# Optimization experiments

Hardware: AMD Instinct MI355X
Metric: run time of the kernel (lower is better)

The kernel has to match this reference:

```python
import jax, jax.numpy as jnp
import numpy as np

B, T, C, H = 4, 2048, 1024, 16
HS = C // H  # head_size = 64
FF = 4 * C   # 4096
EPS = 1e-5


def _layernorm(x, g, b):
    mu = jnp.mean(x, axis=-1, keepdims=True)
    var = jnp.mean(jnp.square(x - mu), axis=-1, keepdims=True)
    return (x - mu) * jax.lax.rsqrt(var + EPS) * g + b


def setup_inputs() -> dict:
    key = jax.random.key(0)
    ks = jax.random.split(key, 12)
    s_in = 1.0 / np.sqrt(C)
    s_ff = 1.0 / np.sqrt(FF)
    return {
        "x": jax.random.normal(ks[0], (B, T, C), jnp.float32),
        # per-head projection weights stacked: [H, C, HS]
        "Wq": jax.random.normal(ks[1], (H, C, HS), jnp.float32) * s_in,
        "Wk": jax.random.normal(ks[2], (H, C, HS), jnp.float32) * s_in,
        "Wv": jax.random.normal(ks[3], (H, C, HS), jnp.float32) * s_in,
        "Wo": jax.random.normal(ks[4], (C, C), jnp.float32) * s_in,
        "bo": jnp.zeros((C,), jnp.float32),
        "g1": jnp.ones((C,), jnp.float32),
        "b1": jnp.zeros((C,), jnp.float32),
        "g2": jnp.ones((C,), jnp.float32),
        "b2": jnp.zeros((C,), jnp.float32),
        "W1": jax.random.normal(ks[5], (C, FF), jnp.float32) * s_in,
        "bf1": jnp.zeros((FF,), jnp.float32),
        "W2": jax.random.normal(ks[6], (FF, C), jnp.float32) * s_ff,
        "bf2": jnp.zeros((C,), jnp.float32),
    }


def reference(x, Wq, Wk, Wv, Wo, bo, g1, b1, g2, b2, W1, bf1, W2, bf2):
    # pre-norm
    h = _layernorm(x, g1, b1)                       # [B,T,C]
    q = jnp.einsum('btc,hcd->bhtd', h, Wq)          # [B,H,T,HS]
    k = jnp.einsum('btc,hcd->bhtd', h, Wk)
    v = jnp.einsum('btc,hcd->bhtd', h, Wv)
    w = jnp.einsum('bhtd,bhsd->bhts', q, k) * (HS ** -0.5)  # [B,H,T,S]
    mask = jnp.tril(jnp.ones((T, T), bool))          # causal tril
    w = jnp.where(mask[None, None], w, -jnp.inf)
    # NB: original code softmaxes over dim=1 of [B,T,T], i.e. the QUERY axis
    w = jax.nn.softmax(w, axis=-2)
    o = jnp.einsum('bhts,bhsd->bhtd', w, v)          # [B,H,T,HS]
    o = jnp.transpose(o, (0, 2, 1, 3)).reshape(B, T, C)  # concat heads
    x = x + o @ Wo + bo                              # residual 1 (dropout=0)
    f = _layernorm(x, g2, b2)
    ff = jax.nn.relu(f @ W1 + bf1) @ W2 + bf2        # FFN (dropout=0)
    return x + ff
```

## Files before the change

### kernel.cpp

```cpp
#include <hip/hip_runtime.h>
#include <hip/hip_bf16.h>


#define T_SEQ 2048
#define SCALE2 0.1803368801f

typedef __attribute__((ext_vector_type(8))) short short8;
typedef __attribute__((ext_vector_type(4))) float f32x4;

typedef __attribute__((address_space(1))) unsigned int g_u32;
typedef __attribute__((address_space(3))) unsigned int l_u32;

__device__ __forceinline__ unsigned short f2bf(float f) {
  __hip_bfloat16 h = __float2bfloat16(f);
  union { __hip_bfloat16 h; unsigned short u; } x; x.h = h;
  return x.u;
}
__device__ __forceinline__ float bf2f(unsigned short u) {
  union { unsigned u; float f; } x; x.u = (unsigned)u << 16;
  return x.f;
}

__device__ __forceinline__ void g2lds16(const void* g, void* l) {
  __builtin_amdgcn_global_load_lds((g_u32*)g, (l_u32*)l, 16, 0, 0);
}

__device__ __forceinline__ int xcd_swz(int flat, int nwg) {
  if ((nwg & 7) != 0) return flat;
  return (flat & 7) * (nwg >> 3) + (flat >> 3);
}

template <int EPI, int BN, int NSTG>
__global__ __launch_bounds__(512, 2) void gemm256(
    const unsigned short* __restrict__ A, const unsigned short* __restrict__ Bt,
    int M, int N, int K,
    unsigned short* __restrict__ out16, float* __restrict__ outF,
    const float* __restrict__ bias, const float* __restrict__ resid) {
  constexpr int PM = (BN == 128) ? 4 : 2;
  constexpr int PN = 8 / PM;
  constexpr int WM = 256 / PM;
  constexpr int FM = WM / 16;
  constexpr int WN = BN / PN;
  constexpr int FN = WN / 16;
  constexpr int NB = (BN * 8) / 512;
  constexpr int NL = 4 + NB;
  extern __shared__ unsigned short lds[];
  unsigned short* ldsA = lds;
  unsigned short* ldsB = lds + NSTG * 16384;
  const int tid = threadIdx.x, lane = tid & 63, wid = tid >> 6;
  const int wm = wid / PN, wn = wid % PN;
  const int nx = gridDim.x;
  const int flat = blockIdx.y * nx + blockIdx.x;
  const int swz = xcd_swz(flat, nx * gridDim.y);
  const int mBase = (swz / nx) * 256, nBase = (swz % nx) * BN;

  f32x4 acc[FM][FN];
#pragma unroll
  for (int i = 0; i < FM; ++i)
#pragma unroll
    for (int j = 0; j < FN; ++j)
#pragma unroll
      for (int e = 0; e < 4; ++e) acc[i][j][e] = 0.f;

  auto stage = [&](int buf, int kt) {
    const int k0 = kt << 6;
#pragma unroll
    for (int it = 0; it < 4; ++it) {
      int g = it * 512 + tid;
      int row = g >> 3, colL = g & 7;
      int col = colL ^ (row & 7);
      g2lds16(A + ((size_t)(mBase + row) * K + k0 + col * 8),
              &ldsA[buf * 16384 + (it * 512 + wid * 64) * 8]);
    }
#pragma unroll
    for (int it = 0; it < NB; ++it) {
      int g = it * 512 + tid;
      int row = g >> 3, colL = g & 7;
      int col = colL ^ (row & 7);
      g2lds16(Bt + ((size_t)(nBase + row) * K + k0 + col * 8),
              &ldsB[buf * (BN * 64) + (it * 512 + wid * 64) * 8]);
    }
  };

  const int nKT = K >> 6;
#pragma unroll
  for (int i = 0; i < NSTG; ++i) stage(i, i);
  asm volatile("s_waitcnt vmcnt(%0)" ::"n"((NSTG - 1) * NL) : "memory");
  __builtin_amdgcn_sched_barrier(0);
  __builtin_amdgcn_s_barrier();
  __builtin_amdgcn_sched_barrier(0);

  for (int kt = 0; kt < nKT; ++kt) {
    const int cur = kt % NSTG;
    short8 bf[FN][2];
#pragma unroll
    for (int fn = 0; fn < FN; ++fn)
#pragma unroll
      for (int ks = 0; ks < 2; ++ks) {
        int r = wn * WN + fn * 16 + (lane & 15);
        int c = (ks * 4 + (lane >> 4)) ^ (r & 7);
        bf[fn][ks] = *(const short8*)&ldsB[cur * (BN * 64) + r * 64 + c * 8];
      }
#pragma unroll
    for (int mf = 0; mf < FM; ++mf) {
      short8 af[2];
#pragma unroll
      for (int ks = 0; ks < 2; ++ks) {
        int r = wm * WM + mf * 16 + (lane & 15);
        int c = (ks * 4 + (lane >> 4)) ^ (r & 7);
        af[ks] = *(const short8*)&ldsA[cur * 16384 + r * 64 + c * 8];
      }
      __builtin_amdgcn_s_setprio(1);
#pragma unroll
      for (int fn = 0; fn < FN; ++fn)
#pragma unroll
        for (int ks = 0; ks < 2; ++ks)
          acc[mf][fn] = __builtin_amdgcn_mfma_f32_16x16x32_bf16(
              af[ks], bf[fn][ks], acc[mf][fn], 0, 0, 0);
      __builtin_amdgcn_s_setprio(0);
    }
    if (kt + 1 < nKT) {
      asm volatile("s_waitcnt lgkmcnt(0)" ::: "memory");
      __builtin_amdgcn_sched_barrier(0);
      __builtin_amdgcn_s_barrier();
      __builtin_amdgcn_sched_barrier(0);
      if (kt + NSTG < nKT) {
        stage(cur, kt + NSTG);
        asm volatile("s_waitcnt vmcnt(%0)" ::"n"((NSTG - 1) * NL) : "memory");
      } else if (NSTG == 3 && kt + 2 < nKT) {
        asm volatile("s_waitcnt vmcnt(%0)" ::"n"(NL) : "memory");
      } else {
        asm volatile("s_waitcnt vmcnt(0)" ::: "memory");
      }
      __builtin_amdgcn_sched_barrier(0);
      __builtin_amdgcn_s_barrier();
      __builtin_amdgcn_sched_barrier(0);
    }
  }

#pragma unroll
  for (int am = 0; am < FM; ++am)
#pragma unroll
    for (int fn = 0; fn < FN; ++fn) {
      int col = nBase + wn * WN + fn * 16 + (lane & 15);
      int row0 = mBase + wm * WM + am * 16 + ((lane >> 4) << 2);
      if (EPI == 0) {
#pragma unroll
        for (int r = 0; r < 4; ++r)
          out16[(size_t)(row0 + r) * N + col] = f2bf(acc[am][fn][r]);
      } else if (EPI == 1) {
        float bv = bias[col];
#pragma unroll
        for (int r = 0; r < 4; ++r) {
          size_t idx = (size_t)(row0 + r) * N + col;
          outF[idx] = acc[am][fn][r] + bv + resid[idx];
        }
      } else {
        float bv = bias[col];
#pragma unroll
        for (int r = 0; r < 4; ++r)
          out16[(size_t)(row0 + r) * N + col] =
              f2bf(fmaxf(acc[am][fn][r] + bv, 0.f));
      }
    }
}

__global__ __launch_bounds__(256) void ln_bf16(
    const float* __restrict__ x, const float* __restrict__ gw,
    const float* __restrict__ bw, unsigned short* __restrict__ out) {
  __shared__ float red[8];
  const int row = blockIdx.x, tid = threadIdx.x;
  const float4 v = ((const float4*)(x + (size_t)row * 1024))[tid];
  float s = v.x + v.y + v.z + v.w;
  float q = v.x * v.x + v.y * v.y + v.z * v.z + v.w * v.w;
#pragma unroll
  for (int off = 32; off >= 1; off >>= 1) {
    s += __shfl_down(s, off);
    q += __shfl_down(q, off);
  }
  const int lane = tid & 63, wid = tid >> 6;
  if (lane == 0) { red[wid] = s; red[4 + wid] = q; }
  __syncthreads();
  float S = red[0] + red[1] + red[2] + red[3];
  float Q = red[4] + red[5] + red[6] + red[7];
  float mu = S * (1.f / 1024.f);
  float var = Q * (1.f / 1024.f) - mu * mu;
  float rs = rsqrtf(var + 1e-5f);
  int c = tid * 4;
  ushort4 ov;
  ov.x = f2bf((v.x - mu) * rs * gw[c + 0] + bw[c + 0]);
  ov.y = f2bf((v.y - mu) * rs * gw[c + 1] + bw[c + 1]);
  ov.z = f2bf((v.z - mu) * rs * gw[c + 2] + bw[c + 2]);
  ov.w = f2bf((v.w - mu) * rs * gw[c + 3] + bw[c + 3]);
  *(ushort4*)&out[(size_t)row * 1024 + c] = ov;
}

__global__ __launch_bounds__(256) void pack_qkv(
    const float* __restrict__ Wq, const float* __restrict__ Wk,
    const float* __restrict__ Wv, unsigned short* __restrict__ out) {
  __shared__ float tile[64 * 65];
  const int tid = threadIdx.x;
  const float* W = (blockIdx.z == 0) ? Wq : (blockIdx.z == 1) ? Wk : Wv;
  const int h = blockIdx.y, r0 = blockIdx.x * 64;
#pragma unroll
  for (int it = 0; it < 4; ++it) {
    int e4 = it * 256 + tid;
    int r = e4 >> 4, c4 = e4 & 15;
    float4 v = *(const float4*)&W[((size_t)h * 1024 + r0 + r) * 64 + c4 * 4];
    tile[r * 65 + c4 * 4 + 0] = v.x;
    tile[r * 65 + c4 * 4 + 1] = v.y;
    tile[r * 65 + c4 * 4 + 2] = v.z;
    tile[r * 65 + c4 * 4 + 3] = v.w;
  }
  __syncthreads();
#pragma unroll
  for (int it = 0; it < 4; ++it) {
    int e4 = it * 256 + tid;
    int d = e4 >> 4, r4 = e4 & 15;
    ushort4 ov;
    ov.x = f2bf(tile[(r4 * 4 + 0) * 65 + d]);
    ov.y = f2bf(tile[(r4 * 4 + 1) * 65 + d]);
    ov.z = f2bf(tile[(r4 * 4 + 2) * 65 + d]);
    ov.w = f2bf(tile[(r4 * 4 + 3) * 65 + d]);
    *(ushort4*)&out[(size_t)(blockIdx.z * 1024 + h * 64 + d) * 1024 + r0 +
                    r4 * 4] = ov;
  }
}

__global__ __launch_bounds__(256) void transpose_cast(
    const float* __restrict__ in, unsigned short* __restrict__ out, int R,
    int C) {
  __shared__ float tile[64 * 65];
  const int tid = threadIdx.x;
  const int r0 = blockIdx.x * 64, c0 = blockIdx.y * 64;
#pragma unroll
  for (int it = 0; it < 4; ++it) {
    int e4 = it * 256 + tid;
    int r = e4 >> 4, c4 = e4 & 15;
    float4 v = *(const float4*)&in[(size_t)(r0 + r) * C + c0 + c4 * 4];
    tile[r * 65 + c4 * 4 + 0] = v.x;
    tile[r * 65 + c4 * 4 + 1] = v.y;
    tile[r * 65 + c4 * 4 + 2] = v.z;
    tile[r * 65 + c4 * 4 + 3] = v.w;
  }
  __syncthreads();
#pragma unroll
  for (int it = 0; it < 4; ++it) {
    int e4 = it * 256 + tid;
    int c = e4 >> 4, r4 = e4 & 15;
    ushort4 ov;
    ov.x = f2bf(tile[(r4 * 4 + 0) * 65 + c]);
    ov.y = f2bf(tile[(r4 * 4 + 1) * 65 + c]);
    ov.z = f2bf(tile[(r4 * 4 + 2) * 65 + c]);
    ov.w = f2bf(tile[(r4 * 4 + 3) * 65 + c]);
    *(ushort4*)&out[(size_t)(c0 + c) * R + r0 + r4 * 4] = ov;
  }
}

__global__ __launch_bounds__(256) void vtrans(
    const unsigned short* __restrict__ qkv, const float* __restrict__ lpart,
    unsigned short* __restrict__ vT) {
  __shared__ unsigned short tile[64 * 66];
  const int tid = threadIdx.x;
  const int bh = blockIdx.y, b = bh >> 4, h = bh & 15;
  const int t0 = blockIdx.x * 64;
#pragma unroll
  for (int it = 0; it < 8; ++it) {
    int e2 = it * 256 + tid;
    int r = e2 >> 5, c2 = e2 & 31;
    unsigned v = *(const unsigned*)&qkv[(size_t)(b * T_SEQ + t0 + r) * 3072 +
                                        2048 + h * 64 + c2 * 2];
    float l0 = lpart[(size_t)bh * T_SEQ + t0 + r];
    float l1 = lpart[(size_t)(64 + bh) * T_SEQ + t0 + r];
    float li = 1.f / (l0 + l1);
    unsigned short lo = f2bf(bf2f((unsigned short)(v & 0xffff)) * li);
    unsigned short hi = f2bf(bf2f((unsigned short)(v >> 16)) * li);
    *(unsigned*)&tile[r * 66 + c2 * 2] = (unsigned)lo | ((unsigned)hi << 16);
  }
  __syncthreads();
#pragma unroll
  for (int it = 0; it < 8; ++it) {
    int e2 = it * 256 + tid;
    int d = e2 >> 5, t2 = e2 & 31;
    unsigned short a = tile[(t2 * 2) * 66 + d];
    unsigned short bb = tile[(t2 * 2 + 1) * 66 + d];
    unsigned pk = (unsigned)a | ((unsigned)bb << 16);
    *(unsigned*)&vT[(size_t)(bh * 64 + d) * T_SEQ + t0 + t2 * 2] = pk;
  }
}

__global__ __launch_bounds__(256, 4) void attn_stats(
    const unsigned short* __restrict__ qkv, float* __restrict__ lpart) {
  __shared__ unsigned short qt[4][2][32 * 64];
  __shared__ float redL[4][2][64];
  const int tid = threadIdx.x, lane = tid & 63, w = tid >> 6;
  const int f = xcd_swz(blockIdx.y * 32 + blockIdx.x, 2048);
  const int half = f & 1, px = (f >> 1) & 15, bh = f >> 5;
  const int b = bh >> 4, h = bh & 15;
  const int sxA = px, sxB = 31 - px;
  const int sA = sxA * 64, sB = sxB * 64;
  const int m = half * 4 + w;

  short8 kfA[4][2], kfB[4][2];
#pragma unroll
  for (int fn = 0; fn < 4; ++fn)
#pragma unroll
    for (int ks = 0; ks < 2; ++ks) {
      int d = 1024 + h * 64 + ks * 32 + ((lane >> 4) << 3);
      kfA[fn][ks] = *(const short8*)&qkv[(size_t)(b * T_SEQ + sA + fn * 16 +
                                                  (lane & 15)) * 3072 + d];
      kfB[fn][ks] = *(const short8*)&qkv[(size_t)(b * T_SEQ + sB + fn * 16 +
                                                  (lane & 15)) * 3072 + d];
    }
  float lA[4] = {0.f, 0.f, 0.f, 0.f}, lB[4] = {0.f, 0.f, 0.f, 0.f};

  auto stageQ = [&](int buf, int idx) {
    int t0 = idx * 32;
#pragma unroll
    for (int it = 0; it < 4; ++it) {
      int g = it * 64 + lane;
      int row = g >> 3;
      int col = (g & 7) ^ (row & 7);
      g2lds16(qkv + ((size_t)(b * T_SEQ + t0 + row) * 3072 + h * 64 + col * 8),
              &qt[w][buf][it * 512]);
    }
  };

  auto accum = [&](const short8 (&af)[2], const short8 (&kf)[4][2],
                   float (&lacc)[4], int sBase, int tRow, bool diag) {
    f32x4 sc[4];
#pragma unroll
    for (int fn = 0; fn < 4; ++fn)
#pragma unroll
      for (int e = 0; e < 4; ++e) sc[fn][e] = 0.f;
    __builtin_amdgcn_s_setprio(1);
#pragma unroll
    for (int fn = 0; fn < 4; ++fn)
#pragma unroll
      for (int ks = 0; ks < 2; ++ks)
        sc[fn] = __builtin_amdgcn_mfma_f32_16x16x32_bf16(af[ks], kf[fn][ks],
                                                         sc[fn], 0, 0, 0);
    __builtin_amdgcn_s_setprio(0);
    if (diag) {
#pragma unroll
      for (int fn = 0; fn < 4; ++fn) {
        int s = sBase + fn * 16 + (lane & 15);
        float e0 = (tRow + 0 >= s) ? exp2f(sc[fn][0] * SCALE2) : 0.f;
        float e1 = (tRow + 1 >= s) ? exp2f(sc[fn][1] * SCALE2) : 0.f;
        float e2 = (tRow + 2 >= s) ? exp2f(sc[fn][2] * SCALE2) : 0.f;
        float e3 = (tRow + 3 >= s) ? exp2f(sc[fn][3] * SCALE2) : 0.f;
        lacc[fn] += (e0 + e1) + (e2 + e3);
      }
    } else {
#pragma unroll
      for (int fn = 0; fn < 4; ++fn) {
        float e0 = exp2f(sc[fn][0] * SCALE2);
        float e1 = exp2f(sc[fn][1] * SCALE2);
        float e2 = exp2f(sc[fn][2] * SCALE2);
        float e3 = exp2f(sc[fn][3] * SCALE2);
        lacc[fn] += (e0 + e1) + (e2 + e3);
      }
    }
  };

  const int d0 = 2 * sxA - m;
  const int fi = m + (d0 > 0 ? (((d0 + 7) >> 3) << 3) : 0);
  int cur = 0;
  if (fi < 64) stageQ(0, fi);
  for (int idx = fi; idx < 64; idx += 8, cur ^= 1) {
    if (idx + 8 < 64) {
      stageQ(cur ^ 1, idx + 8);
      asm volatile("s_waitcnt vmcnt(4)" ::: "memory");
    } else {
      asm volatile("s_waitcnt vmcnt(0)" ::: "memory");
    }
    const int t0g = idx * 32;
    const bool doB = idx >= 2 * sxB;
#pragma unroll
    for (int mf = 0; mf < 2; ++mf) {
      short8 af[2];
#pragma unroll
      for (int ks = 0; ks < 2; ++ks) {
        int r = mf * 16 + (lane & 15);
        int c = (ks * 4 + (lane >> 4)) ^ (r & 7);
        af[ks] = *(const short8*)&qt[w][cur][r * 64 + c * 8];
      }
      int tRow = t0g + mf * 16 + ((lane >> 4) << 2);
      accum(af, kfA, lA, sA, tRow, idx <= 2 * sxA + 1);
      if (doB) accum(af, kfB, lB, sB, tRow, idx <= 2 * sxB + 1);
    }
  }
#pragma unroll
  for (int fn = 0; fn < 4; ++fn) {
    lA[fn] += __shfl_down(lA[fn], 32);
    lA[fn] += __shfl_down(lA[fn], 16);
    lB[fn] += __shfl_down(lB[fn], 32);
    lB[fn] += __shfl_down(lB[fn], 16);
  }
  if (lane < 16) {
#pragma unroll
    for (int fn = 0; fn < 4; ++fn) {
      redL[w][0][fn * 16 + lane] = lA[fn];
      redL[w][1][fn * 16 + lane] = lB[fn];
    }
  }
  __syncthreads();
  if (tid < 128) {
    int which = tid >> 6;
    float l = redL[0][which][lane] + redL[1][which][lane] +
              redL[2][which][lane] + redL[3][which][lane];
    int sbase = (which == 0) ? sA : sB;
    lpart[((size_t)half * 64 + bh) * T_SEQ + sbase + lane] = l;
  }
}

__global__ __launch_bounds__(256, 2) void attn_pv(
    const unsigned short* __restrict__ qkv, const unsigned short* __restrict__ vT,
    unsigned short* __restrict__ o) {
  __shared__ unsigned short kbuf[2][64 * 64];
  __shared__ unsigned short vbuf[2][64 * 64];
  __shared__ unsigned short pl[128 * 64];
  const int tid = threadIdx.x, lane = tid & 63, wid = tid >> 6;
  const int f = xcd_swz(blockIdx.y * 8 + blockIdx.x, 512);
  const int bx = f & 7, bh = f >> 3;
  const int b = bh >> 4, h = bh & 15;
  const int tA = bx * 128, tB = (15 - bx) * 128;
  const int nSTA = 2 * bx + 2, nSTB = 32 - 2 * bx;

  short8 qfA[2][2], qfB[2][2];
#pragma unroll
  for (int mf = 0; mf < 2; ++mf)
#pragma unroll
    for (int ks = 0; ks < 2; ++ks) {
      int d = h * 64 + ks * 32 + ((lane >> 4) << 3);
      int rloc = wid * 32 + mf * 16 + (lane & 15);
      qfA[mf][ks] =
          *(const short8*)&qkv[(size_t)(b * T_SEQ + tA + rloc) * 3072 + d];
      qfB[mf][ks] =
          *(const short8*)&qkv[(size_t)(b * T_SEQ + tB + rloc) * 3072 + d];
    }
  f32x4 oaccA[2][4], oaccB[2][4];
#pragma unroll
  for (int i = 0; i < 2; ++i)
#pragma unroll
    for (int j = 0; j < 4; ++j)
#pragma unroll
      for (int e = 0; e < 4; ++e) { oaccA[i][j][e] = 0.f; oaccB[i][j][e] = 0.f; }

  auto stage = [&](int buf, int st) {
#pragma unroll
    for (int it = 0; it < 2; ++it) {
      int g = it * 256 + tid;
      int row = g >> 3, colL = g & 7;
      int col = colL ^ (row & 7);
      g2lds16(qkv + ((size_t)(b * T_SEQ + st * 64 + row) * 3072 + 1024 +
                     h * 64 + col * 8),
              &kbuf[buf][(it * 256 + wid * 64) * 8]);
      g2lds16(vT + ((size_t)(bh * 64 + row) * T_SEQ + st * 64 + col * 8),
              &vbuf[buf][(it * 256 + wid * 64) * 8]);
    }
  };

  auto qkstore = [&](const short8 (&qf)[2][2], int tBase, int s0,
                     bool maskNeeded, int cur) {
    f32x4 sc[4][2];
#pragma unroll
    for (int i = 0; i < 4; ++i)
#pragma unroll
      for (int j = 0; j < 2; ++j)
#pragma unroll
        for (int e = 0; e < 4; ++e) sc[i][j][e] = 0.f;
    __builtin_amdgcn_s_setprio(1);
#pragma unroll
    for (int fn = 0; fn < 4; ++fn)
#pragma unroll
      for (int ks = 0; ks < 2; ++ks) {
        int r = fn * 16 + (lane & 15);
        int c = (ks * 4 + (lane >> 4)) ^ (r & 7);
        short8 kfr = *(const short8*)&kbuf[cur][r * 64 + c * 8];
        sc[fn][0] = __builtin_amdgcn_mfma_f32_16x16x32_bf16(kfr, qf[0][ks],
                                                            sc[fn][0], 0, 0, 0);
        sc[fn][1] = __builtin_amdgcn_mfma_f32_16x16x32_bf16(kfr, qf[1][ks],
                                                            sc[fn][1], 0, 0, 0);
      }
    __builtin_amdgcn_s_setprio(0);
#pragma unroll
    for (int mf = 0; mf < 2; ++mf) {
      int tl = wid * 32 + mf * 16 + (lane & 15);
      int tG = tBase + tl;
#pragma unroll
      for (int fn = 0; fn < 4; ++fn) {
        int sl = fn * 16 + ((lane >> 4) << 2);
        float p0 = exp2f(sc[fn][mf][0] * SCALE2);
        float p1 = exp2f(sc[fn][mf][1] * SCALE2);
        float p2 = exp2f(sc[fn][mf][2] * SCALE2);
        float p3 = exp2f(sc[fn][mf][3] * SCALE2);
        if (maskNeeded) {
          int sG = s0 + sl;
          p0 = (tG >= sG + 0) ? p0 : 0.f;
          p1 = (tG >= sG + 1) ? p1 : 0.f;
          p2 = (tG >= sG + 2) ? p2 : 0.f;
          p3 = (tG >= sG + 3) ? p3 : 0.f;
        }
        uint2 pk;
        pk.x = (unsigned)f2bf(p0) | ((unsigned)f2bf(p1) << 16);
        pk.y = (unsigned)f2bf(p2) | ((unsigned)f2bf(p3) << 16);
        int byteoff = tl * 128 + ((sl * 2) ^ ((tl & 7) << 4));
        *(uint2*)((char*)pl + byteoff) = pk;
      }
    }
  };

  auto pvphase = [&](f32x4 (&oacc)[2][4], int cur) {
    __builtin_amdgcn_s_setprio(1);
#pragma unroll
    for (int ks = 0; ks < 2; ++ks) {
      short8 pa[2];
#pragma unroll
      for (int mf = 0; mf < 2; ++mf) {
        int rowa = wid * 32 + mf * 16 + (lane & 15);
        int kb = ks * 64 + ((lane >> 4) << 4);
        pa[mf] = *(const short8*)((const char*)pl + rowa * 128 +
                                  (kb ^ ((rowa & 7) << 4)));
      }
#pragma unroll
      for (int df = 0; df < 4; ++df) {
        int r = df * 16 + (lane & 15);
        int c = (ks * 4 + (lane >> 4)) ^ (r & 7);
        short8 vb = *(const short8*)&vbuf[cur][r * 64 + c * 8];
        oacc[0][df] = __builtin_amdgcn_mfma_f32_16x16x32_bf16(pa[0], vb,
                                                              oacc[0][df], 0, 0, 0);
        oacc[1][df] = __builtin_amdgcn_mfma_f32_16x16x32_bf16(pa[1], vb,
                                                              oacc[1][df], 0, 0, 0);
      }
    }
    __builtin_amdgcn_s_setprio(0);
  };

  auto bar_lgkm = [&]() {
    asm volatile("s_waitcnt lgkmcnt(0)" ::: "memory");
    __builtin_amdgcn_sched_barrier(0);
    __builtin_amdgcn_s_barrier();
    __builtin_amdgcn_sched_barrier(0);
  };

  stage(0, 0);
  asm volatile("s_waitcnt vmcnt(0)" ::: "memory");
  __builtin_amdgcn_sched_barrier(0);
  __builtin_amdgcn_s_barrier();
  __builtin_amdgcn_sched_barrier(0);

  int cur = 0;
  for (int st = 0; st < nSTB; ++st) {
    const int s0 = st * 64;
    const bool doA = st < nSTA;

    if (st + 1 < nSTB) stage(cur ^ 1, st + 1);

    if (doA) {
      qkstore(qfA, tA, s0, st >= nSTA - 2, cur);
      bar_lgkm();
      pvphase(oaccA, cur);
      bar_lgkm();
    }
    qkstore(qfB, tB, s0, st >= nSTB - 2, cur);
    bar_lgkm();
    pvphase(oaccB, cur);
    asm volatile("s_waitcnt vmcnt(0) lgkmcnt(0)" ::: "memory");
    __builtin_amdgcn_sched_barrier(0);
    __builtin_amdgcn_s_barrier();
    __builtin_amdgcn_sched_barrier(0);
    cur ^= 1;
  }
#pragma unroll
  for (int mf = 0; mf < 2; ++mf)
#pragma unroll
    for (int df = 0; df < 4; ++df) {
      int d = h * 64 + df * 16 + (lane & 15);
      int ra = tA + wid * 32 + mf * 16 + ((lane >> 4) << 2);
      int rb = tB + wid * 32 + mf * 16 + ((lane >> 4) << 2);
#pragma unroll
      for (int r = 0; r < 4; ++r) {
        o[(size_t)(b * T_SEQ + ra + r) * 1024 + d] = f2bf(oaccA[mf][df][r]);
        o[(size_t)(b * T_SEQ + rb + r) * 1024 + d] = f2bf(oaccB[mf][df][r]);
      }
    }
}

extern "C" void kernel_launch(void* const* d_in, const int* in_sizes, int n_in,
                              void* d_out, int out_size, void* d_ws,
                              size_t ws_size, hipStream_t stream) {
  const float* x = (const float*)d_in[0];
  const float* Wq = (const float*)d_in[1];
  const float* Wk = (const float*)d_in[2];
  const float* Wv = (const float*)d_in[3];
  const float* Wo = (const float*)d_in[4];
  const float* bo = (const float*)d_in[5];
  const float* g1 = (const float*)d_in[6];
  const float* b1 = (const float*)d_in[7];
  const float* g2 = (const float*)d_in[8];
  const float* b2 = (const float*)d_in[9];
  const float* W1 = (const float*)d_in[10];
  const float* bf1 = (const float*)d_in[11];
  const float* W2 = (const float*)d_in[12];
  const float* bf2 = (const float*)d_in[13];
  float* out = (float*)d_out;

  char* ws = (char*)d_ws;
  size_t off = 0;
  auto alloc = [&](size_t bytes) {
    char* p = ws + off;
    off += (bytes + 255) & ~(size_t)255;
    return p;
  };
  unsigned short* Wqkv = (unsigned short*)alloc(3072ull * 1024 * 2);
  unsigned short* WoT = (unsigned short*)alloc(1024ull * 1024 * 2);
  unsigned short* W1T = (unsigned short*)alloc(4096ull * 1024 * 2);
  unsigned short* W2T = (unsigned short*)alloc(1024ull * 4096 * 2);
  unsigned short* hbuf = (unsigned short*)alloc(8192ull * 1024 * 2);
  char* regionE = alloc(8192ull * 3072 * 2 + 64ull * 64 * 2048 * 2);
  unsigned short* qkv = (unsigned short*)regionE;
  unsigned short* vT = (unsigned short*)(regionE + 8192ull * 3072 * 2);
  unsigned short* act = (unsigned short*)regionE;
  float* lbuf = (float*)alloc(128ull * 2048 * 4);
  float* x1 = (float*)alloc(8192ull * 1024 * 4);
  unsigned short* fbuf = (unsigned short*)alloc(8192ull * 1024 * 2);
  unsigned short* obuf = hbuf;

  (void)in_sizes; (void)n_in; (void)out_size; (void)ws_size;

  const size_t LDS128_3 = 3 * (16384 + 8192) * 2;
  const size_t LDS256_2 = 2 * (16384 + 16384) * 2;

  pack_qkv<<<dim3(16, 16, 3), 256, 0, stream>>>(Wq, Wk, Wv, Wqkv);
  transpose_cast<<<dim3(16, 16), 256, 0, stream>>>(Wo, WoT, 1024, 1024);
  transpose_cast<<<dim3(16, 64), 256, 0, stream>>>(W1, W1T, 1024, 4096);
  transpose_cast<<<dim3(64, 16), 256, 0, stream>>>(W2, W2T, 4096, 1024);
  ln_bf16<<<8192, 256, 0, stream>>>(x, g1, b1, hbuf);
  gemm256<0, 128, 3><<<dim3(24, 32), 512, LDS128_3, stream>>>(
      hbuf, Wqkv, 8192, 3072, 1024, qkv, nullptr, nullptr, nullptr);
  attn_stats<<<dim3(32, 64), 256, 0, stream>>>(qkv, lbuf);
  vtrans<<<dim3(32, 64), 256, 0, stream>>>(qkv, lbuf, vT);
  attn_pv<<<dim3(8, 64), 256, 0, stream>>>(qkv, vT, obuf);
  gemm256<1, 128, 3><<<dim3(8, 32), 512, LDS128_3, stream>>>(
      obuf, WoT, 8192, 1024, 1024, nullptr, x1, bo, x);
  ln_bf16<<<8192, 256, 0, stream>>>(x1, g2, b2, fbuf);
  gemm256<2, 256, 2><<<dim3(16, 32), 512, LDS256_2, stream>>>(
      fbuf, W1T, 8192, 4096, 1024, act, nullptr, bf1, nullptr);
  gemm256<1, 128, 3><<<dim3(8, 32), 512, LDS128_3, stream>>>(
      act, W2T, 8192, 1024, 4096, nullptr, out, bf2, x1);
}
```

Before: 435.6 us.

## Split paired causal attention blocks into single-tile blocks and use 2-stage GEMM pipelines

The attn_pv kernel no longer pairs a short and a long causal query tile in one block to balance work. Each block now handles one 128-row query tile, the grid doubles to 1024 blocks, and blocks are ordered longest-first so the scheduler can balance load dynamically. Separately, the 128-wide GEMM instantiations drop from 3 to 2 pipeline stages, which shrinks LDS use and may allow more occupancy at the cost of less latency hiding.

After: 451.2 us. +3.6%, slower.

```diff
diff --git a/kernel.cpp b/kernel.cpp
--- a/kernel.cpp
+++ b/kernel.cpp
@@ -421,31 +421,29 @@
   __shared__ unsigned short vbuf[2][64 * 64];
   __shared__ unsigned short pl[128 * 64];
   const int tid = threadIdx.x, lane = tid & 63, wid = tid >> 6;
-  const int f = xcd_swz(blockIdx.y * 8 + blockIdx.x, 512);
-  const int bx = f & 7, bh = f >> 3;
+  const int f = xcd_swz(blockIdx.y * 16 + blockIdx.x, 1024);
+  const int bx = 15 - (f & 15), bh = f >> 4;
   const int b = bh >> 4, h = bh & 15;
-  const int tA = bx * 128, tB = (15 - bx) * 128;
-  const int nSTA = 2 * bx + 2, nSTB = 32 - 2 * bx;
-
-  short8 qfA[2][2], qfB[2][2];
+  const int tA = bx * 128;
+  const int nST = 2 * bx + 2;
+
+  short8 qf[2][2];
 #pragma unroll
   for (int mf = 0; mf < 2; ++mf)
 #pragma unroll
     for (int ks = 0; ks < 2; ++ks) {
       int d = h * 64 + ks * 32 + ((lane >> 4) << 3);
       int rloc = wid * 32 + mf * 16 + (lane & 15);
-      qfA[mf][ks] =
+      qf[mf][ks] =
           *(const short8*)&qkv[(size_t)(b * T_SEQ + tA + rloc) * 3072 + d];
-      qfB[mf][ks] =
-          *(const short8*)&qkv[(size_t)(b * T_SEQ + tB + rloc) * 3072 + d];
-    }
-  f32x4 oaccA[2][4], oaccB[2][4];
+    }
+  f32x4 oacc[2][4];
 #pragma unroll
   for (int i = 0; i < 2; ++i)
 #pragma unroll
     for (int j = 0; j < 4; ++j)
 #pragma unroll
-      for (int e = 0; e < 4; ++e) { oaccA[i][j][e] = 0.f; oaccB[i][j][e] = 0.f; }
+      for (int e = 0; e < 4; ++e) oacc[i][j][e] = 0.f;
 
   auto stage = [&](int buf, int st) {
 #pragma unroll
@@ -461,8 +459,7 @@
     }
   };
 
-  auto qkstore = [&](const short8 (&qf)[2][2], int tBase, int s0,
-                     bool maskNeeded, int cur) {
+  auto qkstore = [&](int s0, bool maskNeeded, int cur) {
     f32x4 sc[4][2];
 #pragma unroll
     for (int i = 0; i < 4; ++i)
@@ -487,7 +484,7 @@
 #pragma unroll
     for (int mf = 0; mf < 2; ++mf) {
       int tl = wid * 32 + mf * 16 + (lane & 15);
-      int tG = tBase + tl;
+      int tG = tA + tl;
 #pragma unroll
       for (int fn = 0; fn < 4; ++fn) {
         int sl = fn * 16 + ((lane >> 4) << 2);
@@ -511,7 +508,7 @@
     }
   };
 
-  auto pvphase = [&](f32x4 (&oacc)[2][4], int cur) {
+  auto pvphase = [&](int cur) {
     __builtin_amdgcn_s_setprio(1);
 #pragma unroll
     for (int ks = 0; ks < 2; ++ks) {
@@ -537,13 +534,6 @@
     __builtin_amdgcn_s_setprio(0);
   };
 
-  auto bar_lgkm = [&]() {
-    asm volatile("s_waitcnt lgkmcnt(0)" ::: "memory");
-    __builtin_amdgcn_sched_barrier(0);
-    __builtin_amdgcn_s_barrier();
-    __builtin_amdgcn_sched_barrier(0);
-  };
-
   stage(0, 0);
   asm volatile("s_waitcnt vmcnt(0)" ::: "memory");
   __builtin_amdgcn_sched_barrier(0);
@@ -551,21 +541,15 @@
   __builtin_amdgcn_sched_barrier(0);
 
   int cur = 0;
-  for (int st = 0; st < nSTB; ++st) {
-    const int s0 = st * 64;
-    const bool doA = st < nSTA;
-
-    if (st + 1 < nSTB) stage(cur ^ 1, st + 1);
-
-    if (doA) {
-      qkstore(qfA, tA, s0, st >= nSTA - 2, cur);
-      bar_lgkm();
-      pvphase(oaccA, cur);
-      bar_lgkm();
-    }
-    qkstore(qfB, tB, s0, st >= nSTB - 2, cur);
-    bar_lgkm();
-    pvphase(oaccB, cur);
+  for (int st = 0; st < nST; ++st) {
+    if (st + 1 < nST) stage(cur ^ 1, st + 1);
+
+    qkstore(st * 64, st >= nST - 2, cur);
+    asm volatile("s_waitcnt lgkmcnt(0)" ::: "memory");
+    __builtin_amdgcn_sched_barrier(0);
+    __builtin_amdgcn_s_barrier();
+    __builtin_amdgcn_sched_barrier(0);
+    pvphase(cur);
     asm volatile("s_waitcnt vmcnt(0) lgkmcnt(0)" ::: "memory");
     __builtin_amdgcn_sched_barrier(0);
     __builtin_amdgcn_s_barrier();
@@ -578,12 +562,9 @@
     for (int df = 0; df < 4; ++df) {
       int d = h * 64 + df * 16 + (lane & 15);
       int ra = tA + wid * 32 + mf * 16 + ((lane >> 4) << 2);
-      int rb = tB + wid * 32 + mf * 16 + ((lane >> 4) << 2);
-#pragma unroll
-      for (int r = 0; r < 4; ++r) {
-        o[(size_t)(b * T_SEQ + ra + r) * 1024 + d] = f2bf(oaccA[mf][df][r]);
-        o[(size_t)(b * T_SEQ + rb + r) * 1024 + d] = f2bf(oaccB[mf][df][r]);
-      }
+#pragma unroll
+      for (int r = 0; r < 4; ++r)
+        o[(size_t)(b * T_SEQ + ra + r) * 1024 + d] = f2bf(oacc[mf][df][r]);
     }
 }
 
@@ -629,7 +610,7 @@
 
   (void)in_sizes; (void)n_in; (void)out_size; (void)ws_size;
 
-  const size_t LDS128_3 = 3 * (16384 + 8192) * 2;
+  const size_t LDS128_2 = 2 * (16384 + 8192) * 2;
   const size_t LDS256_2 = 2 * (16384 + 16384) * 2;
 
   pack_qkv<<<dim3(16, 16, 3), 256, 0, stream>>>(Wq, Wk, Wv, Wqkv);
@@ -637,16 +618,16 @@
   transpose_cast<<<dim3(16, 64), 256, 0, stream>>>(W1, W1T, 1024, 4096);
   transpose_cast<<<dim3(64, 16), 256, 0, stream>>>(W2, W2T, 4096, 1024);
   ln_bf16<<<8192, 256, 0, stream>>>(x, g1, b1, hbuf);
-  gemm256<0, 128, 3><<<dim3(24, 32), 512, LDS128_3, stream>>>(
+  gemm256<0, 128, 2><<<dim3(24, 32), 512, LDS128_2, stream>>>(
       hbuf, Wqkv, 8192, 3072, 1024, qkv, nullptr, nullptr, nullptr);
   attn_stats<<<dim3(32, 64), 256, 0, stream>>>(qkv, lbuf);
   vtrans<<<dim3(32, 64), 256, 0, stream>>>(qkv, lbuf, vT);
-  attn_pv<<<dim3(8, 64), 256, 0, stream>>>(qkv, vT, obuf);
-  gemm256<1, 128, 3><<<dim3(8, 32), 512, LDS128_3, stream>>>(
+  attn_pv<<<dim3(16, 64), 256, 0, stream>>>(qkv, vT, obuf);
+  gemm256<1, 128, 2><<<dim3(8, 32), 512, LDS128_2, stream>>>(
       obuf, WoT, 8192, 1024, 1024, nullptr, x1, bo, x);
   ln_bf16<<<8192, 256, 0, stream>>>(x1, g2, b2, fbuf);
   gemm256<2, 256, 2><<<dim3(16, 32), 512, LDS256_2, stream>>>(
       fbuf, W1T, 8192, 4096, 1024, act, nullptr, bf1, nullptr);
-  gemm256<1, 128, 3><<<dim3(8, 32), 512, LDS128_3, stream>>>(
+  gemm256<1, 128, 2><<<dim3(8, 32), 512, LDS128_2, stream>>>(
       act, W2T, 8192, 1024, 4096, nullptr, out, bf2, x1);
 }
```
